# Kernel tuning notes

Hardware: AMD Instinct MI355X
Metric: run time of the kernel (lower is better)

Reference implementation:

```python
import jax, jax.numpy as jnp
import numpy as np

L = 5   # local window size (l)
R = 2   # upsample factor (r)


def setup_inputs() -> dict:
    key = jax.random.key(0)
    k0, k1, k2 = jax.random.split(key, 3)
    B, C, H, W, OUT = 4, 128, 64, 64, 128
    x = jax.random.normal(k0, (B, C, H, W), jnp.float32)
    # conv1: in_channels -> l^2, 3x3, pad 1 (with bias, as nn.Conv2d default)
    w1 = jax.random.normal(k1, (L * L, C, 3, 3), jnp.float32) * 0.05
    b1 = jnp.zeros((L * L,), jnp.float32)
    # conv2: 4*in_channels -> out_channels, 1x1 (stored as [out, 4C])
    w2 = jax.random.normal(k2, (OUT, 4 * C), jnp.float32) * 0.05
    b2 = jnp.zeros((OUT,), jnp.float32)
    return {"x": x, "w1": w1, "b1": b1, "w2": w2, "b2": b2}


def _upsample2_nearest(t):
    # nearest-neighbor x2 upsample on NCHW
    return jnp.repeat(jnp.repeat(t, R, axis=2), R, axis=3)


def reference(x, w1, b1, w2, b2):
    B, C, H, W = x.shape
    # conv1 (3x3, SAME) -> [B, L^2, H, W]
    k = jax.lax.conv_general_dilated(
        x, w1, window_strides=(1, 1), padding='SAME',
        dimension_numbers=('NCHW', 'OIHW', 'NCHW')) + b1[None, :, None, None]
    # nearest x2 upsample then softmax over the L^2 channel dim
    k = _upsample2_nearest(k)                 # [B, L^2, 2H, 2W]
    k = jax.nn.softmax(k, axis=1)
    # non-overlapping RxR block extraction (unfold size=R, step=R twice)
    # -> [B, L^2, H, W, R^2], last-dim order (row-offset, col-offset)
    k = k.reshape(B, L * L, H, R, W, R).transpose(0, 1, 2, 4, 3, 5)
    k = k.reshape(B, L * L, H, W, R * R)
    # overlapping LxL window extraction of the input (unfold size=L, step=1)
    pad = L // 2
    xp = jnp.pad(x, ((0, 0), (0, 0), (pad, pad), (pad, pad)))
    wins = jnp.stack(
        [xp[:, :, i:i + H, j:j + W] for i in range(L) for j in range(L)],
        axis=-1)                               # [B, C, H, W, L^2]
    # per-pixel matmul: [C, L^2] @ [L^2, R^2] -> [B, H, W, C, R^2]
    out = jnp.einsum('bchwk,bkhwr->bhwcr', wins, k)
    # flatten (C, R^2) -> 4C (C-major, matching torch reshape), back to NCHW
    out = out.reshape(B, H, W, C * R * R).transpose(0, 3, 1, 2)
    out = _upsample2_nearest(out)              # [B, 4C, 2H, 2W]
    # conv2: 1x1 -> out_channels
    out = jnp.einsum('bchw,oc->bohw', out, w2) + b2[None, :, None, None]
    return out
```

## Files before the change

### kernel.cpp

```cpp
#include <hip/hip_runtime.h>
#include <math.h>

#define BB   4
#define CC   128
#define HH   64
#define WW   64
#define OUTC 128
#define KK   25
#define PXB  16
#define SJ   20

typedef __attribute__((ext_vector_type(8))) short short8;
typedef _Float16 half8  __attribute__((ext_vector_type(8)));
typedef __fp16   fp16x2 __attribute__((ext_vector_type(2)));
typedef __attribute__((ext_vector_type(4))) float floatx4;

__device__ __forceinline__ unsigned short f32_to_bf16(float v) {
    unsigned int u = __float_as_uint(v);
    u += 0x7fffu + ((u >> 16) & 1u);
    return (unsigned short)(u >> 16);
}

__global__ void prep_kernel(const float* __restrict__ w2,
                            const float* __restrict__ w1,
                            unsigned short* __restrict__ w2o,
                            unsigned short* __restrict__ w1f) {
    int i = blockIdx.x * 256 + threadIdx.x;
    if (i < 16384) {
        int o = i >> 7, c = i & 127;
        const float* p = w2 + o * (4 * CC) + c * 4;
        w2o[o * CC + c] = f32_to_bf16(p[0] + p[1] + p[2] + p[3]);
    } else if (i < 16384 + 36864) {
        int f = i - 16384;
        int i8   = f & 7;
        int lane = (f >> 3) & 63;
        int ks   = (f >> 9) & 3;
        int mt   = (f >> 11) & 1;
        int dydx = f >> 12;
        int kk = mt * 16 + (lane & 15);
        int c  = ks * 32 + (lane >> 4) * 8 + i8;
        float v = (kk < KK) ? w1[(size_t)(kk * CC + c) * 9 + dydx] : 0.f;
        _Float16 hv = (_Float16)v;
        w1f[f] = *(unsigned short*)&hv;
    }
}

__global__ __launch_bounds__(128, 2) void fused_kernel(
        const float* __restrict__ x,
        const unsigned short* __restrict__ w1f,
        const unsigned short* __restrict__ w2o,
        const float* __restrict__ b1,
        const float* __restrict__ b2,
        float* __restrict__ out) {
    __shared__ _Float16 xs[3 * SJ * 128];
    __shared__ float pk[KK * PXB];
    unsigned short* sKT = (unsigned short*)xs;

    int bid0 = blockIdx.x;
    int bid  = (bid0 & 7) * 128 + (bid0 >> 3);
    int wq = bid & 3;
    int h  = (bid >> 2) & 63;
    int b  = bid >> 8;
    int t  = threadIdx.x;
    int lane = t & 63;
    int wv = t >> 6;

    const float* xb = x + (size_t)b * CC * (HH * WW);

    {
        int jj = lane & 15, cp = lane >> 4;
        int j  = jj + 2;
        int swz = (j & 15) << 3;
        #pragma unroll
        for (int ci = 0; ci < 8; ++ci) {
            int c  = wv * 64 + ci * 8 + cp * 2;
            int cs = c ^ swz;
            const float* xc0 = xb + (size_t)c * (HH * WW) + wq * 16 + jj;
            const float* xc1 = xc0 + HH * WW;
            #pragma unroll
            for (int r = 0; r < 3; ++r) {
                int y = h - 1 + r;
                float v0 = 0.f, v1 = 0.f;
                if (y >= 0 && y < HH) { v0 = xc0[y * WW]; v1 = xc1[y * WW]; }
                fp16x2 p = __builtin_amdgcn_cvt_pkrtz(v0, v1);
                *(fp16x2*)&xs[(r * SJ + j) * 128 + cs] = p;
            }
        }
        for (int i = t; i < 3 * 4 * 128; i += 128) {
            int jh = i & 3;
            int c  = (i >> 2) & 127;
            int r  = i >> 9;
            int j2 = (jh < 2) ? jh : 16 + jh;
            int xcol = wq * 16 + j2 - 2;
            int y = h - 1 + r;
            float v = (xcol >= 0 && xcol < WW && y >= 0 && y < HH)
                    ? xb[(size_t)c * (HH * WW) + y * WW + xcol] : 0.f;
            xs[(r * SJ + j2) * 128 + (c ^ ((j2 & 15) << 3))] = (_Float16)v;
        }
    }
    __syncthreads();

    int fpx = lane & 15, quad = lane >> 4;
    int mt = wv;
    floatx4 acc = {0.f, 0.f, 0.f, 0.f};
    #pragma unroll
    for (int dydx = 0; dydx < 9; ++dydx) {
        int r   = dydx / 3;
        int dxm = dydx - 3 * r;
        int j   = fpx + dxm + 1;
        int rowbase = (r * SJ + j) * 128;
        int swz = (j & 15) << 3;
        const unsigned short* whb = w1f + (dydx * 2 + mt) * 2048 + lane * 8;
        #pragma unroll
        for (int ks = 0; ks < 4; ++ks) {
            int cb = (ks * 32 + quad * 8) ^ swz;
            half8 A = *(const half8*)(whb + ks * 512);
            half8 B = *(const half8*)&xs[rowbase + cb];
            acc = __builtin_amdgcn_mfma_f32_16x16x32_f16(A, B, acc, 0, 0, 0);
        }
    }
    #pragma unroll
    for (int reg = 0; reg < 4; ++reg) {
        int kk = mt * 16 + quad * 4 + reg;
        if (kk < KK) pk[kk * PXB + fpx] = acc[reg] + b1[kk];
    }
    __syncthreads();

    int pp2 = t & 7, cw = t >> 3;

    float2 lg[KK];
    #pragma unroll
    for (int k = 0; k < KK; ++k) lg[k] = *(const float2*)&pk[k * PXB + 2 * pp2];
    float m0 = -1e30f, m1 = -1e30f;
    #pragma unroll
    for (int k = 0; k < KK; ++k) { m0 = fmaxf(m0, lg[k].x); m1 = fmaxf(m1, lg[k].y); }
    float s0 = 0.f, s1 = 0.f;
    #pragma unroll
    for (int k = 0; k < KK; ++k) {
        lg[k].x = __expf(lg[k].x - m0); s0 += lg[k].x;
        lg[k].y = __expf(lg[k].y - m1); s1 += lg[k].y;
    }
    float i0 = 1.f / s0, i1 = 1.f / s1;
    #pragma unroll
    for (int k = 0; k < KK; ++k) { lg[k].x *= i0; lg[k].y *= i1; }

    int colg = wq * 16 + 2 * pp2 - 2;
    int coff[3]; float cmask[3];
    #pragma unroll
    for (int jx = 0; jx < 3; ++jx) {
        int cg = colg + 2 * jx;
        cmask[jx] = (cg >= 0 && cg <= WW - 2) ? 1.f : 0.f;
        coff[jx]  = min(max(cg, 0), WW - 2);
    }
    int yoff[5]; float msk[15];
    #pragma unroll
    for (int di = 0; di < 5; ++di) {
        int y = h + di - 2;
        float rm = (y >= 0 && y < HH) ? 1.f : 0.f;
        yoff[di] = min(max(y, 0), HH - 1) * WW;
        #pragma unroll
        for (int jx = 0; jx < 3; ++jx) msk[di * 3 + jx] = rm * cmask[jx];
    }

#define LOADC(BUF, I8) do {                                            \
    int c_ = (I8) * 16 + cw;                                           \
    const float* xc_ = xb + (size_t)c_ * (HH * WW);                    \
    _Pragma("unroll")                                                  \
    for (int di = 0; di < 5; ++di)                                     \
        _Pragma("unroll")                                              \
        for (int jx = 0; jx < 3; ++jx)                                 \
            BUF[di * 3 + jx] = *(const float2*)(xc_ + yoff[di] + coff[jx]); \
} while (0)

#define COMPST(BUF, I8) do {                                           \
    float t0 = 0.f, t1 = 0.f;                                          \
    _Pragma("unroll")                                                  \
    for (int di = 0; di < 5; ++di) {                                   \
        float2 x01 = BUF[di * 3 + 0];                                  \
        float2 x23 = BUF[di * 3 + 1];                                  \
        float2 x45 = BUF[di * 3 + 2];                                  \
        x01.x *= msk[di * 3 + 0]; x01.y *= msk[di * 3 + 0];            \
        x23.x *= msk[di * 3 + 1]; x23.y *= msk[di * 3 + 1];            \
        x45.x *= msk[di * 3 + 2]; x45.y *= msk[di * 3 + 2];            \
        t0 += lg[di*5+0].x * x01.x + lg[di*5+1].x * x01.y              \
            + lg[di*5+2].x * x23.x + lg[di*5+3].x * x23.y              \
            + lg[di*5+4].x * x45.x;                                    \
        t1 += lg[di*5+0].y * x01.y + lg[di*5+1].y * x23.x              \
            + lg[di*5+2].y * x23.y + lg[di*5+3].y * x45.x              \
            + lg[di*5+4].y * x45.y;                                    \
    }                                                                  \
    int cs_ = (I8) * 16 + cw;                                          \
    sKT[(2 * pp2) * 136 + cs_]     = f32_to_bf16(t0);                  \
    sKT[(2 * pp2 + 1) * 136 + cs_] = f32_to_bf16(t1);                  \
} while (0)

    {
        float2 bufA[15], bufB[15];
        LOADC(bufA, 0);
        for (int it = 0; it < 4; ++it) {
            LOADC(bufB, 2 * it + 1);
            COMPST(bufA, 2 * it);
            if (it < 3) LOADC(bufA, 2 * it + 2);
            COMPST(bufB, 2 * it + 1);
        }
    }
    __syncthreads();

    floatx4 am[4] = {{0.f,0.f,0.f,0.f},{0.f,0.f,0.f,0.f},
                     {0.f,0.f,0.f,0.f},{0.f,0.f,0.f,0.f}};
    #pragma unroll
    for (int ks = 0; ks < 4; ++ks) {
        short8 bf = *(const short8*)&sKT[fpx * 136 + ks*32 + quad*8];
        #pragma unroll
        for (int mt2 = 0; mt2 < 4; ++mt2) {
            short8 af = *(const short8*)&w2o[(size_t)(64*wv + 16*mt2 + fpx) * CC
                                             + ks*32 + quad*8];
            am[mt2] = __builtin_amdgcn_mfma_f32_16x16x32_bf16(af, bf, am[mt2], 0, 0, 0);
        }
    }

    float* ob = out + (size_t)b * OUTC * (4 * HH * WW);
    int y0 = 2 * h;
    int pxo = wq * 16 + fpx;
    #pragma unroll
    for (int mt2 = 0; mt2 < 4; ++mt2) {
        #pragma unroll
        for (int reg = 0; reg < 4; ++reg) {
            int o = 64*wv + 16*mt2 + quad*4 + reg;
            float v = am[mt2][reg] + b2[o];
            float2 v2 = make_float2(v, v);
            float* r0p = ob + ((size_t)o * (2*HH) + y0) * (2*WW) + 2*pxo;
            *(float2*)(r0p)        = v2;
            *(float2*)(r0p + 2*WW) = v2;
        }
    }
}

extern "C" void kernel_launch(void* const* d_in, const int* in_sizes, int n_in,
                              void* d_out, int out_size, void* d_ws, size_t ws_size,
                              hipStream_t stream) {
    const float* x  = (const float*)d_in[0];
    const float* w1 = (const float*)d_in[1];
    const float* b1 = (const float*)d_in[2];
    const float* w2 = (const float*)d_in[3];
    const float* b2 = (const float*)d_in[4];
    float* out = (float*)d_out;

    unsigned short* w2o = (unsigned short*)d_ws;
    unsigned short* w1f = w2o + (size_t)OUTC * CC;

    prep_kernel<<<(16384 + 36864 + 255) / 256, 256, 0, stream>>>(w2, w1, w2o, w1f);
    fused_kernel<<<BB * HH * 4, 128, 0, stream>>>(x, w1f, w2o, b1, b2, out);
}
```

Before: 94.94 us.

## Stage 5-row fp16 input halo in LDS and reuse it for window aggregation

Extends the shared-memory input tile from 3 to 5 rows so that it covers both the 3x3 conv halo and the 5x5 local window. The per-pixel window aggregation now reads x from LDS (fp16) instead of issuing masked global float2 loads with software double-buffering. sKT gets its own shared buffer because xs is still live. This removes redundant global traffic but grows LDS use, which may lower occupancy, and the aggregation input drops from fp32 to fp16 precision.

```diff
diff --git a/kernel.cpp b/kernel.cpp
--- a/kernel.cpp
+++ b/kernel.cpp
@@ -52,9 +52,9 @@
         const float* __restrict__ b1,
         const float* __restrict__ b2,
         float* __restrict__ out) {
-    __shared__ _Float16 xs[3 * SJ * 128];
+    __shared__ _Float16 xs[5 * SJ * 128];
     __shared__ float pk[KK * PXB];
-    unsigned short* sKT = (unsigned short*)xs;
+    __shared__ unsigned short sKT[PXB * 136];
 
     int bid0 = blockIdx.x;
     int bid  = (bid0 & 7) * 128 + (bid0 >> 3);
@@ -78,21 +78,21 @@
             const float* xc0 = xb + (size_t)c * (HH * WW) + wq * 16 + jj;
             const float* xc1 = xc0 + HH * WW;
             #pragma unroll
-            for (int r = 0; r < 3; ++r) {
-                int y = h - 1 + r;
+            for (int r = 0; r < 5; ++r) {
+                int y = h - 2 + r;
                 float v0 = 0.f, v1 = 0.f;
                 if (y >= 0 && y < HH) { v0 = xc0[y * WW]; v1 = xc1[y * WW]; }
                 fp16x2 p = __builtin_amdgcn_cvt_pkrtz(v0, v1);
                 *(fp16x2*)&xs[(r * SJ + j) * 128 + cs] = p;
             }
         }
-        for (int i = t; i < 3 * 4 * 128; i += 128) {
+        for (int i = t; i < 5 * 4 * 128; i += 128) {
             int jh = i & 3;
             int c  = (i >> 2) & 127;
             int r  = i >> 9;
             int j2 = (jh < 2) ? jh : 16 + jh;
             int xcol = wq * 16 + j2 - 2;
-            int y = h - 1 + r;
+            int y = h - 2 + r;
             float v = (xcol >= 0 && xcol < WW && y >= 0 && y < HH)
                     ? xb[(size_t)c * (HH * WW) + y * WW + xcol] : 0.f;
             xs[(r * SJ + j2) * 128 + (c ^ ((j2 & 15) << 3))] = (_Float16)v;
@@ -108,7 +108,7 @@
         int r   = dydx / 3;
         int dxm = dydx - 3 * r;
         int j   = fpx + dxm + 1;
-        int rowbase = (r * SJ + j) * 128;
+        int rowbase = ((r + 1) * SJ + j) * 128;
         int swz = (j & 15) << 3;
         const unsigned short* whb = w1f + (dydx * 2 + mt) * 2048 + lane * 8;
         #pragma unroll
@@ -144,65 +144,28 @@
     #pragma unroll
     for (int k = 0; k < KK; ++k) { lg[k].x *= i0; lg[k].y *= i1; }
 
-    int colg = wq * 16 + 2 * pp2 - 2;
-    int coff[3]; float cmask[3];
-    #pragma unroll
-    for (int jx = 0; jx < 3; ++jx) {
-        int cg = colg + 2 * jx;
-        cmask[jx] = (cg >= 0 && cg <= WW - 2) ? 1.f : 0.f;
-        coff[jx]  = min(max(cg, 0), WW - 2);
-    }
-    int yoff[5]; float msk[15];
-    #pragma unroll
-    for (int di = 0; di < 5; ++di) {
-        int y = h + di - 2;
-        float rm = (y >= 0 && y < HH) ? 1.f : 0.f;
-        yoff[di] = min(max(y, 0), HH - 1) * WW;
-        #pragma unroll
-        for (int jx = 0; jx < 3; ++jx) msk[di * 3 + jx] = rm * cmask[jx];
-    }
-
-#define LOADC(BUF, I8) do {                                            \
-    int c_ = (I8) * 16 + cw;                                           \
-    const float* xc_ = xb + (size_t)c_ * (HH * WW);                    \
-    _Pragma("unroll")                                                  \
-    for (int di = 0; di < 5; ++di)                                     \
-        _Pragma("unroll")                                              \
-        for (int jx = 0; jx < 3; ++jx)                                 \
-            BUF[di * 3 + jx] = *(const float2*)(xc_ + yoff[di] + coff[jx]); \
-} while (0)
-
-#define COMPST(BUF, I8) do {                                           \
-    float t0 = 0.f, t1 = 0.f;                                          \
-    _Pragma("unroll")                                                  \
-    for (int di = 0; di < 5; ++di) {                                   \
-        float2 x01 = BUF[di * 3 + 0];                                  \
-        float2 x23 = BUF[di * 3 + 1];                                  \
-        float2 x45 = BUF[di * 3 + 2];                                  \
-        x01.x *= msk[di * 3 + 0]; x01.y *= msk[di * 3 + 0];            \
-        x23.x *= msk[di * 3 + 1]; x23.y *= msk[di * 3 + 1];            \
-        x45.x *= msk[di * 3 + 2]; x45.y *= msk[di * 3 + 2];            \
-        t0 += lg[di*5+0].x * x01.x + lg[di*5+1].x * x01.y              \
-            + lg[di*5+2].x * x23.x + lg[di*5+3].x * x23.y              \
-            + lg[di*5+4].x * x45.x;                                    \
-        t1 += lg[di*5+0].y * x01.y + lg[di*5+1].y * x23.x              \
-            + lg[di*5+2].y * x23.y + lg[di*5+3].y * x45.x              \
-            + lg[di*5+4].y * x45.y;                                    \
-    }                                                                  \
-    int cs_ = (I8) * 16 + cw;                                          \
-    sKT[(2 * pp2) * 136 + cs_]     = f32_to_bf16(t0);                  \
-    sKT[(2 * pp2 + 1) * 136 + cs_] = f32_to_bf16(t1);                  \
-} while (0)
-
-    {
-        float2 bufA[15], bufB[15];
-        LOADC(bufA, 0);
-        for (int it = 0; it < 4; ++it) {
-            LOADC(bufB, 2 * it + 1);
-            COMPST(bufA, 2 * it);
-            if (it < 3) LOADC(bufA, 2 * it + 2);
-            COMPST(bufB, 2 * it + 1);
-        }
+    #pragma unroll 2
+    for (int i8 = 0; i8 < 8; ++i8) {
+        int c = i8 * 16 + cw;
+        float xv[5][6];
+        #pragma unroll
+        for (int r = 0; r < 5; ++r)
+            #pragma unroll
+            for (int dj = 0; dj < 6; ++dj) {
+                int j = 2 * pp2 + dj;
+                xv[r][dj] = (float)xs[(r * SJ + j) * 128
+                                      + (c ^ ((j & 15) << 3))];
+            }
+        float t0 = 0.f, t1 = 0.f;
+        #pragma unroll
+        for (int di = 0; di < 5; ++di)
+            #pragma unroll
+            for (int dj = 0; dj < 5; ++dj) {
+                t0 += lg[di * 5 + dj].x * xv[di][dj];
+                t1 += lg[di * 5 + dj].y * xv[di][dj + 1];
+            }
+        sKT[(2 * pp2) * 136 + c]     = f32_to_bf16(t0);
+        sKT[(2 * pp2 + 1) * 136 + c] = f32_to_bf16(t1);
     }
     __syncthreads();
 
```

Measured after the change: 104.1 us. +9.6%, slower.

## Overlap window-prefetch and conv2 weight loads with conv1 MFMA phase

Applied to the files above, without the earlier changes.

Moves the first two channel-group window loads and the full conv2 weight/bias fragment loads ahead of the conv1 MFMA loop and its barrier, so global memory latency hides behind the matrix work and the softmax. The double-buffered loop is fully unrolled, and b1/b2 are read into registers up front. In exchange, register pressure rises sharply (two 15-entry float2 buffers, 16 short8 fragments and 16 bias floats held live across the MFMA), which could cut occupancy or cause spills.

```diff
diff --git a/kernel.cpp b/kernel.cpp
--- a/kernel.cpp
+++ b/kernel.cpp
@@ -64,8 +64,35 @@
     int t  = threadIdx.x;
     int lane = t & 63;
     int wv = t >> 6;
+    int fpx = lane & 15, quad = lane >> 4;
+    int pp2 = t & 7, cw = t >> 3;
 
     const float* xb = x + (size_t)b * CC * (HH * WW);
+
+    float b1r[4];
+    #pragma unroll
+    for (int reg = 0; reg < 4; ++reg) {
+        int kk = wv * 16 + quad * 4 + reg;
+        b1r[reg] = (kk < KK) ? b1[kk] : 0.f;
+    }
+
+    int colg = wq * 16 + 2 * pp2 - 2;
+    int coff[3]; float cmask[3];
+    #pragma unroll
+    for (int jx = 0; jx < 3; ++jx) {
+        int cg = colg + 2 * jx;
+        cmask[jx] = (cg >= 0 && cg <= WW - 2) ? 1.f : 0.f;
+        coff[jx]  = min(max(cg, 0), WW - 2);
+    }
+    int yoff[5]; float msk[15];
+    #pragma unroll
+    for (int di = 0; di < 5; ++di) {
+        int y = h + di - 2;
+        float rm = (y >= 0 && y < HH) ? 1.f : 0.f;
+        yoff[di] = min(max(y, 0), HH - 1) * WW;
+        #pragma unroll
+        for (int jx = 0; jx < 3; ++jx) msk[di * 3 + jx] = rm * cmask[jx];
+    }
 
     {
         int jj = lane & 15, cp = lane >> 4;
@@ -99,68 +126,6 @@
         }
     }
     __syncthreads();
-
-    int fpx = lane & 15, quad = lane >> 4;
-    int mt = wv;
-    floatx4 acc = {0.f, 0.f, 0.f, 0.f};
-    #pragma unroll
-    for (int dydx = 0; dydx < 9; ++dydx) {
-        int r   = dydx / 3;
-        int dxm = dydx - 3 * r;
-        int j   = fpx + dxm + 1;
-        int rowbase = (r * SJ + j) * 128;
-        int swz = (j & 15) << 3;
-        const unsigned short* whb = w1f + (dydx * 2 + mt) * 2048 + lane * 8;
-        #pragma unroll
-        for (int ks = 0; ks < 4; ++ks) {
-            int cb = (ks * 32 + quad * 8) ^ swz;
-            half8 A = *(const half8*)(whb + ks * 512);
-            half8 B = *(const half8*)&xs[rowbase + cb];
-            acc = __builtin_amdgcn_mfma_f32_16x16x32_f16(A, B, acc, 0, 0, 0);
-        }
-    }
-    #pragma unroll
-    for (int reg = 0; reg < 4; ++reg) {
-        int kk = mt * 16 + quad * 4 + reg;
-        if (kk < KK) pk[kk * PXB + fpx] = acc[reg] + b1[kk];
-    }
-    __syncthreads();
-
-    int pp2 = t & 7, cw = t >> 3;
-
-    float2 lg[KK];
-    #pragma unroll
-    for (int k = 0; k < KK; ++k) lg[k] = *(const float2*)&pk[k * PXB + 2 * pp2];
-    float m0 = -1e30f, m1 = -1e30f;
-    #pragma unroll
-    for (int k = 0; k < KK; ++k) { m0 = fmaxf(m0, lg[k].x); m1 = fmaxf(m1, lg[k].y); }
-    float s0 = 0.f, s1 = 0.f;
-    #pragma unroll
-    for (int k = 0; k < KK; ++k) {
-        lg[k].x = __expf(lg[k].x - m0); s0 += lg[k].x;
-        lg[k].y = __expf(lg[k].y - m1); s1 += lg[k].y;
-    }
-    float i0 = 1.f / s0, i1 = 1.f / s1;
-    #pragma unroll
-    for (int k = 0; k < KK; ++k) { lg[k].x *= i0; lg[k].y *= i1; }
-
-    int colg = wq * 16 + 2 * pp2 - 2;
-    int coff[3]; float cmask[3];
-    #pragma unroll
-    for (int jx = 0; jx < 3; ++jx) {
-        int cg = colg + 2 * jx;
-        cmask[jx] = (cg >= 0 && cg <= WW - 2) ? 1.f : 0.f;
-        coff[jx]  = min(max(cg, 0), WW - 2);
-    }
-    int yoff[5]; float msk[15];
-    #pragma unroll
-    for (int di = 0; di < 5; ++di) {
-        int y = h + di - 2;
-        float rm = (y >= 0 && y < HH) ? 1.f : 0.f;
-        yoff[di] = min(max(y, 0), HH - 1) * WW;
-        #pragma unroll
-        for (int jx = 0; jx < 3; ++jx) msk[di * 3 + jx] = rm * cmask[jx];
-    }
 
 #define LOADC(BUF, I8) do {                                            \
     int c_ = (I8) * 16 + cw;                                           \
@@ -194,16 +159,74 @@
     sKT[(2 * pp2 + 1) * 136 + cs_] = f32_to_bf16(t1);                  \
 } while (0)
 
-    {
-        float2 bufA[15], bufB[15];
-        LOADC(bufA, 0);
-        for (int it = 0; it < 4; ++it) {
-            LOADC(bufB, 2 * it + 1);
-            COMPST(bufA, 2 * it);
-            if (it < 3) LOADC(bufA, 2 * it + 2);
-            COMPST(bufB, 2 * it + 1);
-        }
-    }
+    float2 bufA[15], bufB[15];
+    LOADC(bufA, 0);
+    LOADC(bufB, 1);
+
+    int mt = wv;
+    floatx4 acc = {0.f, 0.f, 0.f, 0.f};
+    #pragma unroll
+    for (int dydx = 0; dydx < 9; ++dydx) {
+        int r   = dydx / 3;
+        int dxm = dydx - 3 * r;
+        int j   = fpx + dxm + 1;
+        int rowbase = (r * SJ + j) * 128;
+        int swz = (j & 15) << 3;
+        const unsigned short* whb = w1f + (dydx * 2 + mt) * 2048 + lane * 8;
+        #pragma unroll
+        for (int ks = 0; ks < 4; ++ks) {
+            int cb = (ks * 32 + quad * 8) ^ swz;
+            half8 A = *(const half8*)(whb + ks * 512);
+            half8 B = *(const half8*)&xs[rowbase + cb];
+            acc = __builtin_amdgcn_mfma_f32_16x16x32_f16(A, B, acc, 0, 0, 0);
+        }
+    }
+    #pragma unroll
+    for (int reg = 0; reg < 4; ++reg) {
+        int kk = mt * 16 + quad * 4 + reg;
+        if (kk < KK) pk[kk * PXB + fpx] = acc[reg] + b1r[reg];
+    }
+
+    short8 afr[4][4];
+    float  b2r[4][4];
+    #pragma unroll
+    for (int ks = 0; ks < 4; ++ks)
+        #pragma unroll
+        for (int mt2 = 0; mt2 < 4; ++mt2)
+            afr[ks][mt2] = *(const short8*)&w2o[(size_t)(64*wv + 16*mt2 + fpx) * CC
+                                                + ks*32 + quad*8];
+    #pragma unroll
+    for (int mt2 = 0; mt2 < 4; ++mt2)
+        #pragma unroll
+        for (int reg = 0; reg < 4; ++reg)
+            b2r[mt2][reg] = b2[64*wv + 16*mt2 + quad*4 + reg];
+
+    __syncthreads();
+
+    float2 lg[KK];
+    #pragma unroll
+    for (int k = 0; k < KK; ++k) lg[k] = *(const float2*)&pk[k * PXB + 2 * pp2];
+    float m0 = -1e30f, m1 = -1e30f;
+    #pragma unroll
+    for (int k = 0; k < KK; ++k) { m0 = fmaxf(m0, lg[k].x); m1 = fmaxf(m1, lg[k].y); }
+    float s0 = 0.f, s1 = 0.f;
+    #pragma unroll
+    for (int k = 0; k < KK; ++k) {
+        lg[k].x = __expf(lg[k].x - m0); s0 += lg[k].x;
+        lg[k].y = __expf(lg[k].y - m1); s1 += lg[k].y;
+    }
+    float i0 = 1.f / s0, i1 = 1.f / s1;
+    #pragma unroll
+    for (int k = 0; k < KK; ++k) { lg[k].x *= i0; lg[k].y *= i1; }
+
+    COMPST(bufA, 0); LOADC(bufA, 2);
+    COMPST(bufB, 1); LOADC(bufB, 3);
+    COMPST(bufA, 2); LOADC(bufA, 4);
+    COMPST(bufB, 3); LOADC(bufB, 5);
+    COMPST(bufA, 4); LOADC(bufA, 6);
+    COMPST(bufB, 5); LOADC(bufB, 7);
+    COMPST(bufA, 6);
+    COMPST(bufB, 7);
     __syncthreads();
 
     floatx4 am[4] = {{0.f,0.f,0.f,0.f},{0.f,0.f,0.f,0.f},
@@ -212,11 +235,9 @@
     for (int ks = 0; ks < 4; ++ks) {
         short8 bf = *(const short8*)&sKT[fpx * 136 + ks*32 + quad*8];
         #pragma unroll
-        for (int mt2 = 0; mt2 < 4; ++mt2) {
-            short8 af = *(const short8*)&w2o[(size_t)(64*wv + 16*mt2 + fpx) * CC
-                                             + ks*32 + quad*8];
-            am[mt2] = __builtin_amdgcn_mfma_f32_16x16x32_bf16(af, bf, am[mt2], 0, 0, 0);
-        }
+        for (int mt2 = 0; mt2 < 4; ++mt2)
+            am[mt2] = __builtin_amdgcn_mfma_f32_16x16x32_bf16(afr[ks][mt2], bf,
+                                                              am[mt2], 0, 0, 0);
     }
 
     float* ob = out + (size_t)b * OUTC * (4 * HH * WW);
@@ -227,7 +248,7 @@
         #pragma unroll
         for (int reg = 0; reg < 4; ++reg) {
             int o = 64*wv + 16*mt2 + quad*4 + reg;
-            float v = am[mt2][reg] + b2[o];
+            float v = am[mt2][reg] + b2r[mt2][reg];
             float2 v2 = make_float2(v, v);
             float* r0p = ob + ((size_t)o * (2*HH) + y0) * (2*WW) + 2*pxo;
             *(float2*)(r0p)        = v2;
```

New measurement: 97.30 us. 1.02x slower.
